# Performance work log

Hardware: AMD Instinct MI355X
Metric: run time of the kernel (lower is better)

The kernel has to match this reference:

```python
import jax, jax.numpy as jnp
import numpy as np

B, L, R, D = 4, 1024, 4, 1024   # batch, seq, expansion rate, model dim
HEADS, HD, FF = 16, 64, 4096
EPS = 1e-6


def _static_alpha(layer_id):
    a0 = np.zeros((R, 1), np.float32)
    a0[layer_id % R, 0] = 1.0
    return jnp.asarray(np.concatenate([a0, np.eye(R, dtype=np.float32)], axis=1))  # [R, R+1]


def setup_inputs() -> dict:
    key = jax.random.key(0)
    ks = jax.random.split(key, 12)
    w = lambda k, shape, s=0.02: (jax.random.normal(k, shape, jnp.float32) * s)
    return {
        "H": jax.random.normal(ks[0], (B, L, R, D), jnp.float32),
        # attention hyper-connection (layer_id*2 = 0)
        "hc1_norm_w": jnp.ones((D,), jnp.float32),
        "hc1_alpha_fn": w(ks[1], (D, R + 1), 0.01),
        "hc1_beta_fn": w(ks[2], (D,), 0.01),
        "hc1_a_scale": jnp.full((1,), 0.01, jnp.float32),
        "hc1_b_scale": jnp.full((1,), 0.01, jnp.float32),
        "hc1_s_alpha": _static_alpha(0),
        "hc1_s_beta": jnp.ones((R,), jnp.float32),
        # attention
        "attn_norm_w": jnp.ones((D,), jnp.float32),
        "qkv_w": w(ks[3], (3 * D, D)),
        "out_w": w(ks[4], (D, D)),
        # ffn hyper-connection (layer_id*2+1 = 1)
        "hc2_norm_w": jnp.ones((D,), jnp.float32),
        "hc2_alpha_fn": w(ks[5], (D, R + 1), 0.01),
        "hc2_beta_fn": w(ks[6], (D,), 0.01),
        "hc2_a_scale": jnp.full((1,), 0.01, jnp.float32),
        "hc2_b_scale": jnp.full((1,), 0.01, jnp.float32),
        "hc2_s_alpha": _static_alpha(1),
        "hc2_s_beta": jnp.ones((R,), jnp.float32),
        # ffn
        "ffn_norm_w": jnp.ones((D,), jnp.float32),
        "fc1_w": w(ks[7], (FF, D)),
        "fc2_w": w(ks[8], (D, FF)),
    }


def _rms(x, weight):
    norm = jnp.sqrt(jnp.mean(x * x, axis=-1, keepdims=True))
    return weight * x / (norm + EPS)


def _width(Hm, norm_w, alpha_fn, beta_fn, a_scale, b_scale, s_alpha, s_beta):
    nh = _rms(Hm, norm_w)                                      # [B,L,R,D]
    alpha = jnp.tanh(jnp.einsum('blnd,dk->blnk', nh, alpha_fn)) * a_scale + s_alpha  # [B,L,R,R+1]
    beta = jnp.tanh(jnp.einsum('blnd,d->bln', nh, beta_fn)) * b_scale + s_beta       # [B,L,R]
    mix = jnp.einsum('blnk,blnd->blkd', alpha, Hm)             # [B,L,R+1,D]
    return mix, beta


def _depth(mix, out, beta):
    return beta[..., None] * out[:, :, None, :] + mix[..., 1:, :]


def _attention(x, qkv_w, out_w):
    b, l, d = x.shape
    qkv = (x @ qkv_w.T).reshape(b, l, 3, HEADS, HD)
    q, k, v = (jnp.moveaxis(qkv, 2, 0)[i].transpose(0, 2, 1, 3) for i in range(3))  # [B,H,L,HD]
    scores = jnp.einsum('bhqd,bhkd->bhqk', q, k) * (HD ** -0.5)
    causal = jnp.tril(jnp.ones((l, l), bool))
    scores = jnp.where(causal, scores, jnp.float32(-jnp.inf))
    attn = jax.nn.softmax(scores, axis=-1)
    out = jnp.einsum('bhqk,bhkd->bhqd', attn, v).transpose(0, 2, 1, 3).reshape(b, l, d)
    return out @ out_w.T


def reference(H, hc1_norm_w, hc1_alpha_fn, hc1_beta_fn, hc1_a_scale, hc1_b_scale,
              hc1_s_alpha, hc1_s_beta, attn_norm_w, qkv_w, out_w,
              hc2_norm_w, hc2_alpha_fn, hc2_beta_fn, hc2_a_scale, hc2_b_scale,
              hc2_s_alpha, hc2_s_beta, ffn_norm_w, fc1_w, fc2_w):
    # attention block
    mix, beta = _width(H, hc1_norm_w, hc1_alpha_fn, hc1_beta_fn,
                       hc1_a_scale, hc1_b_scale, hc1_s_alpha, hc1_s_beta)
    h = _rms(mix[..., 0, :], attn_norm_w)
    h = _attention(h, qkv_w, out_w)
    H = _depth(mix, h, beta)
    # ffn block
    mix, beta = _width(H, hc2_norm_w, hc2_alpha_fn, hc2_beta_fn,
                       hc2_a_scale, hc2_b_scale, hc2_s_alpha, hc2_s_beta)
    h = _rms(mix[..., 0, :], ffn_norm_w)
    h = (jax.nn.gelu(h @ fc1_w.T, approximate=False)) @ fc2_w.T
    H = _depth(mix, h, beta)
    return H
```

## Files before the change

### kernel.cpp

```cpp
#include <hip/hip_runtime.h>
#include <math.h>

#define BB 4
#define LL 1024
#define RR 4
#define DD 1024
#define NHEADS 16
#define HDIM 64
#define FFD 4096
#define EPSV 1e-6f

typedef short s16x8 __attribute__((ext_vector_type(8)));
typedef float f32x4 __attribute__((ext_vector_type(4)));
typedef unsigned short u16;

__device__ inline unsigned short f2bf(float x) {
  unsigned u = __builtin_bit_cast(unsigned, x);
  unsigned r = (u + 0x7fffu + ((u >> 16) & 1u)) >> 16;
  return (unsigned short)r;
}
__device__ inline float bf2f(u16 x) {
  return __builtin_bit_cast(float, (unsigned)x << 16);
}

__device__ inline float wred_sum(float v) {
#pragma unroll
  for (int off = 32; off; off >>= 1) v += __shfl_down(v, off);
  return v;
}

__device__ inline void gload_lds16(const u16* g, u16* l) {
  __builtin_amdgcn_global_load_lds(
      (const __attribute__((address_space(1))) unsigned int*)g,
      (__attribute__((address_space(3))) unsigned int*)l, 16, 0, 0);
}

__global__ __launch_bounds__(256) void cvt4_kernel(
    const float* __restrict__ s0, const float* __restrict__ s1,
    const float* __restrict__ s2, const float* __restrict__ s3,
    u16* __restrict__ d0, u16* __restrict__ d1,
    u16* __restrict__ d2, u16* __restrict__ d3) {
  const int n0 = 786432, n1 = 262144, n2 = 1048576, n3 = 1048576;
  const int total = n0 + n1 + n2 + n3;
  for (int i = blockIdx.x * 256 + threadIdx.x; i < total; i += gridDim.x * 256) {
    const float4* src; ushort4* dst; int j;
    if (i < n0)                { src = (const float4*)s0; dst = (ushort4*)d0; j = i; }
    else if (i < n0 + n1)      { src = (const float4*)s1; dst = (ushort4*)d1; j = i - n0; }
    else if (i < n0 + n1 + n2) { src = (const float4*)s2; dst = (ushort4*)d2; j = i - n0 - n1; }
    else                       { src = (const float4*)s3; dst = (ushort4*)d3; j = i - n0 - n1 - n2; }
    float4 v = src[j];
    ushort4 o;
    o.x = f2bf(v.x); o.y = f2bf(v.y); o.z = f2bf(v.z); o.w = f2bf(v.w);
    dst[j] = o;
  }
}

template<int NP>
__global__ __launch_bounds__(256) void width_kernel(
    const float* __restrict__ Hin,
    const u16* mixrest_in,
    const float* __restrict__ beta_in,
    const u16* __restrict__ pp,
    const float* __restrict__ hc_norm_w,
    const float* __restrict__ alpha_fn,
    const float* __restrict__ beta_fn,
    const float* __restrict__ a_scale,
    const float* __restrict__ b_scale,
    const float* __restrict__ s_alpha,
    const float* __restrict__ s_beta,
    const float* __restrict__ post_norm_w,
    u16* mixrest_out,
    float* __restrict__ beta_out,
    u16* __restrict__ x_out)
{
  const size_t MN = (size_t)4096 * 1024;
  const int bl = blockIdx.x;
  const int t = threadIdx.x;
  const int wid = t >> 6;
  __shared__ __align__(16) float Hs[4 * 1024];
  __shared__ __align__(16) float m0[1024];
  __shared__ float scr[96];
  __shared__ float alpha_s[4][5];
  __shared__ float beta_s[4];
  __shared__ float inv_s[4];
  __shared__ float inv0_s;

  if (NP > 0) {
    int d0 = t * 4;
    float4 s; s.x = 0.f; s.y = 0.f; s.z = 0.f; s.w = 0.f;
#pragma unroll
    for (int p = 0; p < (NP > 0 ? NP : 1); ++p) {
      ushort4 v = *(const ushort4*)&pp[p * MN + (size_t)bl * 1024 + d0];
      s.x += bf2f(v.x); s.y += bf2f(v.y); s.z += bf2f(v.z); s.w += bf2f(v.w);
    }
    ((float4*)m0)[t] = s;
    __syncthreads();
    for (int i = t; i < 1024; i += 256) {
      int n = i >> 8;
      float be = beta_in[bl * 4 + n];
      ushort4 mr = ((const ushort4*)(mixrest_in + (size_t)bl * 4096))[i];
      float4 ao = ((const float4*)m0)[i & 255];
      float4 hv;
      hv.x = be * ao.x + bf2f(mr.x); hv.y = be * ao.y + bf2f(mr.y);
      hv.z = be * ao.z + bf2f(mr.z); hv.w = be * ao.w + bf2f(mr.w);
      ((float4*)Hs)[i] = hv;
    }
  } else {
    for (int i = t; i < 1024; i += 256)
      ((float4*)Hs)[i] = ((const float4*)(Hin + (size_t)bl * 4096))[i];
  }
  __syncthreads();

  float ss[4];
#pragma unroll
  for (int n = 0; n < 4; ++n) {
    float a = 0.f;
    for (int d = t; d < 1024; d += 256) { float v = Hs[n * 1024 + d]; a += v * v; }
    ss[n] = a;
  }
#pragma unroll
  for (int n = 0; n < 4; ++n) {
    float r = wred_sum(ss[n]);
    if ((t & 63) == 0) scr[wid * 4 + n] = r;
  }
  __syncthreads();
  if (t < 4) {
    float tot = scr[t] + scr[4 + t] + scr[8 + t] + scr[12 + t];
    inv_s[t] = 1.f / (sqrtf(tot * (1.f / 1024.f)) + EPSV);
  }
  __syncthreads();
  float inv[4] = {inv_s[0], inv_s[1], inv_s[2], inv_s[3]};

  float dots[4][6];
#pragma unroll
  for (int n = 0; n < 4; ++n)
#pragma unroll
    for (int k = 0; k < 6; ++k) dots[n][k] = 0.f;
  for (int d = t; d < 1024; d += 256) {
    float w = hc_norm_w[d];
    float a0 = alpha_fn[d * 5 + 0], a1 = alpha_fn[d * 5 + 1], a2 = alpha_fn[d * 5 + 2],
          a3 = alpha_fn[d * 5 + 3], a4 = alpha_fn[d * 5 + 4];
    float bfv = beta_fn[d];
#pragma unroll
    for (int n = 0; n < 4; ++n) {
      float nh = Hs[n * 1024 + d] * w * inv[n];
      dots[n][0] += nh * a0; dots[n][1] += nh * a1; dots[n][2] += nh * a2;
      dots[n][3] += nh * a3; dots[n][4] += nh * a4; dots[n][5] += nh * bfv;
    }
  }
  __syncthreads();
#pragma unroll
  for (int n = 0; n < 4; ++n)
#pragma unroll
    for (int k = 0; k < 6; ++k) {
      float r = wred_sum(dots[n][k]);
      if ((t & 63) == 0) scr[wid * 24 + n * 6 + k] = r;
    }
  __syncthreads();
  if (t < 24) {
    float raw = scr[t] + scr[24 + t] + scr[48 + t] + scr[72 + t];
    int n = t / 6, k = t % 6;
    if (k < 5) alpha_s[n][k] = tanhf(raw) * a_scale[0] + s_alpha[n * 5 + k];
    else       beta_s[n]     = tanhf(raw) * b_scale[0] + s_beta[n];
  }
  __syncthreads();

  {
    int i = t;
    float4 h0 = ((const float4*)Hs)[i];
    float4 h1 = ((const float4*)Hs)[256 + i];
    float4 h2 = ((const float4*)Hs)[512 + i];
    float4 h3 = ((const float4*)Hs)[768 + i];
#pragma unroll
    for (int k = 0; k < 5; ++k) {
      float c0 = alpha_s[0][k], c1 = alpha_s[1][k], c2 = alpha_s[2][k], c3 = alpha_s[3][k];
      float4 mv;
      mv.x = c0 * h0.x + c1 * h1.x + c2 * h2.x + c3 * h3.x;
      mv.y = c0 * h0.y + c1 * h1.y + c2 * h2.y + c3 * h3.y;
      mv.z = c0 * h0.z + c1 * h1.z + c2 * h2.z + c3 * h3.z;
      mv.w = c0 * h0.w + c1 * h1.w + c2 * h2.w + c3 * h3.w;
      if (k == 0) {
        ((float4*)m0)[i] = mv;
      } else {
        ushort4 ov;
        ov.x = f2bf(mv.x); ov.y = f2bf(mv.y); ov.z = f2bf(mv.z); ov.w = f2bf(mv.w);
        ((ushort4*)(mixrest_out + (size_t)bl * 4096 + (size_t)(k - 1) * 1024))[i] = ov;
      }
    }
  }
  if (t < 4) beta_out[bl * 4 + t] = beta_s[t];
  __syncthreads();

  {
    float a = 0.f;
    for (int d = t; d < 1024; d += 256) { float v = m0[d]; a += v * v; }
    float r = wred_sum(a);
    if ((t & 63) == 0) scr[wid] = r;
  }
  __syncthreads();
  if (t == 0) {
    float tot = scr[0] + scr[1] + scr[2] + scr[3];
    inv0_s = 1.f / (sqrtf(tot * (1.f / 1024.f)) + EPSV);
  }
  __syncthreads();
  {
    float iv = inv0_s;
    float4 mv = ((const float4*)m0)[t];
    float4 wv = ((const float4*)post_norm_w)[t];
    ushort4 ov;
    ov.x = f2bf(wv.x * mv.x * iv);
    ov.y = f2bf(wv.y * mv.y * iv);
    ov.z = f2bf(wv.z * mv.z * iv);
    ov.w = f2bf(wv.w * mv.w * iv);
    ((ushort4*)(x_out + (size_t)bl * 1024))[t] = ov;
  }
}

template<int EPI, int SPLIT>
__global__ __launch_bounds__(256, 4) void gemm_bt_kernel(
    const u16* __restrict__ A, const u16* __restrict__ W,
    u16* __restrict__ Cb, u16* __restrict__ Vt,
    int M, int N, int K)
{
  __shared__ __align__(16) u16 LDSb[2][2][128 * 32];
  const int tn = N >> 7, tm = M >> 7;
  int bid = blockIdx.x;
  const int nwg = gridDim.x;
  if ((nwg & 7) == 0) bid = (bid & 7) * (nwg >> 3) + (bid >> 3);
  const int ts = tm * tn;
  const int sK = bid / ts;
  const int tb = bid - sK * ts;
  const int bm = tb / tn, bn = tb % tn;
  const int Kc = K / SPLIT;
  const int kbeg = sK * Kc;

  const int t = threadIdx.x, l = t & 63, w = t >> 6;
  const int wr = w >> 1, wc = w & 1;
  const int m0 = bm << 7, n0 = bn << 7;
  const int ssc = (((l & 3) ^ ((l >> 3) & 3)) << 3);
  const int srA = m0 + (w << 5) + (l >> 2);
  const int srB = n0 + (w << 5) + (l >> 2);
  const int ldso = (w << 10);
  const int fr = l & 15, g4 = l >> 4;
  const int fc8 = ((g4 ^ ((l >> 1) & 3)) << 3);

  f32x4 acc[4][4];
#pragma unroll
  for (int i = 0; i < 4; ++i)
#pragma unroll
    for (int j = 0; j < 4; ++j)
#pragma unroll
      for (int e = 0; e < 4; ++e) acc[i][j][e] = 0.f;

  const u16* pa0 = A + (size_t)srA * K + kbeg + ssc;
  const u16* pa1 = A + (size_t)(srA + 16) * K + kbeg + ssc;
  const u16* pb0 = W + (size_t)srB * K + kbeg + ssc;
  const u16* pb1 = W + (size_t)(srB + 16) * K + kbeg + ssc;

#define STAGE(buf, koff)                                   \
  do {                                                     \
    gload_lds16(pa0 + (koff), &LDSb[buf][0][ldso]);        \
    gload_lds16(pa1 + (koff), &LDSb[buf][0][ldso + 512]);  \
    gload_lds16(pb0 + (koff), &LDSb[buf][1][ldso]);        \
    gload_lds16(pb1 + (koff), &LDSb[buf][1][ldso + 512]);  \
  } while (0)

  const int nt = Kc >> 5;
  STAGE(0, 0);
  int cur = 0;
  for (int kt = 0; kt < nt; ++kt) {
    if (kt + 1 < nt) {
      STAGE(cur ^ 1, (kt + 1) << 5);
      asm volatile("s_waitcnt vmcnt(4)" ::: "memory");
    } else {
      asm volatile("s_waitcnt vmcnt(0)" ::: "memory");
    }
    __builtin_amdgcn_s_barrier();
    __builtin_amdgcn_sched_barrier(0);
    s16x8 af[4], bfr[4];
#pragma unroll
    for (int m = 0; m < 4; ++m)
      af[m] = *(const s16x8*)(&LDSb[cur][0][(wr * 64 + m * 16 + fr) * 32 + fc8]);
#pragma unroll
    for (int n = 0; n < 4; ++n)
      bfr[n] = *(const s16x8*)(&LDSb[cur][1][(wc * 64 + n * 16 + fr) * 32 + fc8]);
#pragma unroll
    for (int m = 0; m < 4; ++m)
#pragma unroll
      for (int n = 0; n < 4; ++n)
        acc[m][n] = __builtin_amdgcn_mfma_f32_16x16x32_bf16(af[m], bfr[n], acc[m][n], 0, 0, 0);
    asm volatile("s_waitcnt lgkmcnt(0)" ::: "memory");
    __builtin_amdgcn_sched_barrier(0);
    __builtin_amdgcn_s_barrier();
    cur ^= 1;
  }
#undef STAGE

  if (EPI == 2 && n0 >= 2048) {
    const int rbv = m0 + wr * 64 + (g4 << 2);
    const int cbv = n0 + wc * 64 + fr;
#pragma unroll
    for (int m = 0; m < 4; ++m)
#pragma unroll
      for (int n = 0; n < 4; ++n) {
        int cc = cbv + n * 16 - 2048;
        int hh = cc >> 6, dd = cc & 63;
        int r0 = rbv + m * 16;
        ushort4 ov;
        ov.x = f2bf(acc[m][n][0]); ov.y = f2bf(acc[m][n][1]);
        ov.z = f2bf(acc[m][n][2]); ov.w = f2bf(acc[m][n][3]);
        *(ushort4*)&Vt[((size_t)((r0 >> 10) * 16 + hh) * 64 + dd) * 1024 + (r0 & 1023)] = ov;
      }
    return;
  }

  float* scr = (float*)LDSb;
  const int strideN = (EPI == 2) ? 2048 : N;
  u16* Cout = (SPLIT > 1) ? (Cb + (size_t)sK * M * N) : Cb;
#pragma unroll
  for (int r = 0; r < 2; ++r) {
    __syncthreads();
    if (wr == r) {
#pragma unroll
      for (int m = 0; m < 4; ++m)
#pragma unroll
        for (int n = 0; n < 4; ++n)
#pragma unroll
          for (int j = 0; j < 4; ++j) {
            int lr = m * 16 + (g4 << 2) + j;
            int col = wc * 64 + n * 16 + fr;
            scr[lr * 128 + (col ^ ((((lr >> 2) & 7)) << 3))] = acc[m][n][j];
          }
    }
    __syncthreads();
#pragma unroll
    for (int it = 0; it < 4; ++it) {
      int lr = it * 16 + (t >> 4);
      int key8 = ((lr >> 2) & 7) << 3;
      int lc = (t & 15) << 3;
      int cb0 = (lc ^ key8);
      f32x4 v0 = *(const f32x4*)&scr[lr * 128 + cb0];
      f32x4 v1 = *(const f32x4*)&scr[lr * 128 + cb0 + 4];
      float vv[8] = {v0[0], v0[1], v0[2], v0[3], v1[0], v1[1], v1[2], v1[3]};
      s16x8 ov;
#pragma unroll
      for (int c = 0; c < 8; ++c) {
        float v = vv[c];
        if (EPI == 1) v = 0.5f * v * (1.f + erff(v * 0.70710678118f));
        ov[c] = (short)f2bf(v);
      }
      size_t gr = (size_t)(m0 + r * 64 + lr);
      *(s16x8*)&Cout[gr * strideN + n0 + lc] = ov;
    }
  }
}

__global__ __launch_bounds__(256) void attn_mfma_kernel(
    const u16* __restrict__ qk, const u16* __restrict__ Vt, u16* __restrict__ out)
{
  const int h = blockIdx.y, b = blockIdx.z;
  const int qt = (h & 1) ? (15 - blockIdx.x) : blockIdx.x;
  const int t = threadIdx.x, l = t & 63, w = t >> 6;
  const int q0 = qt << 6;
  __shared__ __align__(16) u16 Ks[64 * 64];
  __shared__ __align__(16) u16 Vs[64 * 64];
  __shared__ __align__(16) u16 Ps[4][16 * 64];

  const int fr = l & 15;
  const int fg = (l >> 4) << 3;
  const int fswz = (fr & 7) << 3;

  const int qrow = q0 + w * 16 + fr;
  const size_t qbase = (size_t)(b * 1024 + qrow) * 2048 + h * 64 + fg;
  const s16x8 aq0 = *(const s16x8*)(qk + qbase);
  const s16x8 aq1 = *(const s16x8*)(qk + qbase + 32);

  f32x4 acc_o[4];
#pragma unroll
  for (int i = 0; i < 4; ++i)
#pragma unroll
    for (int e = 0; e < 4; ++e) acc_o[i][e] = 0.f;
  float m_i[4] = {-INFINITY, -INFINITY, -INFINITY, -INFINITY};
  float l_i[4] = {0.f, 0.f, 0.f, 0.f};

  const int srow = t >> 2;
  const int sc = (t & 3) << 4;
  const int c0s = sc ^ ((srow & 7) << 3);
  const int c1s = (sc + 8) ^ ((srow & 7) << 3);
  const int qrow_c = q0 + w * 16 + ((l >> 4) << 2);
  u16* Psw = &Ps[w][0];
  const int nkt = qt + 1;

  for (int kt = 0; kt < nkt; ++kt) {
    const int kb = kt << 6;
    __syncthreads();
    {
      size_t kg = (size_t)(b * 1024 + kb + srow) * 2048 + 1024 + h * 64 + sc;
      s16x8 kv0 = *(const s16x8*)(qk + kg);
      s16x8 kv1 = *(const s16x8*)(qk + kg + 8);
      size_t vg = (size_t)((b * 16 + h) * 64 + srow) * 1024 + kb + sc;
      s16x8 vv0 = *(const s16x8*)(Vt + vg);
      s16x8 vv1 = *(const s16x8*)(Vt + vg + 8);
      *(s16x8*)(Ks + srow * 64 + c0s) = kv0;
      *(s16x8*)(Ks + srow * 64 + c1s) = kv1;
      *(s16x8*)(Vs + srow * 64 + c0s) = vv0;
      *(s16x8*)(Vs + srow * 64 + c1s) = vv1;
    }
    __syncthreads();

    f32x4 s[4];
#pragma unroll
    for (int n = 0; n < 4; ++n) {
#pragma unroll
      for (int e = 0; e < 4; ++e) s[n][e] = 0.f;
      s16x8 bk0 = *(const s16x8*)(Ks + (n * 16 + fr) * 64 + (fg ^ fswz));
      s16x8 bk1 = *(const s16x8*)(Ks + (n * 16 + fr) * 64 + ((32 + fg) ^ fswz));
      s[n] = __builtin_amdgcn_mfma_f32_16x16x32_bf16(aq0, bk0, s[n], 0, 0, 0);
      s[n] = __builtin_amdgcn_mfma_f32_16x16x32_bf16(aq1, bk1, s[n], 0, 0, 0);
    }
#pragma unroll
    for (int n = 0; n < 4; ++n)
#pragma unroll
      for (int e = 0; e < 4; ++e) s[n][e] *= 0.125f;
    if (kt == qt) {
#pragma unroll
      for (int n = 0; n < 4; ++n) {
        int kc = kb + n * 16 + fr;
#pragma unroll
        for (int r = 0; r < 4; ++r)
          if (kc > qrow_c + r) s[n][r] = -INFINITY;
      }
    }

    float rm[4], fac[4];
#pragma unroll
    for (int r = 0; r < 4; ++r)
      rm[r] = fmaxf(fmaxf(s[0][r], s[1][r]), fmaxf(s[2][r], s[3][r]));
#pragma unroll
    for (int off = 1; off < 16; off <<= 1)
#pragma unroll
      for (int r = 0; r < 4; ++r) rm[r] = fmaxf(rm[r], __shfl_xor(rm[r], off));
#pragma unroll
    for (int r = 0; r < 4; ++r) {
      float mn = fmaxf(m_i[r], rm[r]);
      fac[r] = __expf(m_i[r] - mn);
      m_i[r] = mn;
    }
    float rs[4] = {0.f, 0.f, 0.f, 0.f};
    float pb[4][4];
#pragma unroll
    for (int n = 0; n < 4; ++n)
#pragma unroll
      for (int r = 0; r < 4; ++r) {
        float pv = __expf(s[n][r] - m_i[r]);
        pb[n][r] = pv;
        rs[r] += pv;
      }
#pragma unroll
    for (int off = 1; off < 16; off <<= 1)
#pragma unroll
      for (int r = 0; r < 4; ++r) rs[r] += __shfl_xor(rs[r], off);
#pragma unroll
    for (int r = 0; r < 4; ++r) l_i[r] = l_i[r] * fac[r] + rs[r];
#pragma unroll
    for (int dt = 0; dt < 4; ++dt)
#pragma unroll
      for (int r = 0; r < 4; ++r) acc_o[dt][r] *= fac[r];

#pragma unroll
    for (int n = 0; n < 4; ++n)
#pragma unroll
      for (int r = 0; r < 4; ++r) {
        int prow = ((l >> 4) << 2) + r;
        Psw[prow * 64 + ((n * 16 + fr) ^ ((prow & 7) << 3))] = f2bf(pb[n][r]);
      }
    asm volatile("s_waitcnt lgkmcnt(0)" ::: "memory");
    __builtin_amdgcn_sched_barrier(0);

    s16x8 pa0 = *(const s16x8*)(Psw + fr * 64 + (fg ^ fswz));
    s16x8 pa1 = *(const s16x8*)(Psw + fr * 64 + ((32 + fg) ^ fswz));
#pragma unroll
    for (int dt = 0; dt < 4; ++dt) {
      s16x8 bv0 = *(const s16x8*)(Vs + (dt * 16 + fr) * 64 + (fg ^ fswz));
      s16x8 bv1 = *(const s16x8*)(Vs + (dt * 16 + fr) * 64 + ((32 + fg) ^ fswz));
      acc_o[dt] = __builtin_amdgcn_mfma_f32_16x16x32_bf16(pa0, bv0, acc_o[dt], 0, 0, 0);
      acc_o[dt] = __builtin_amdgcn_mfma_f32_16x16x32_bf16(pa1, bv1, acc_o[dt], 0, 0, 0);
    }
  }

  float invl[4];
#pragma unroll
  for (int r = 0; r < 4; ++r) invl[r] = 1.f / l_i[r];
#pragma unroll
  for (int dt = 0; dt < 4; ++dt)
#pragma unroll
    for (int r = 0; r < 4; ++r) {
      size_t idx = (size_t)(b * 1024 + qrow_c + r) * 1024 + h * 64 + dt * 16 + fr;
      out[idx] = f2bf(acc_o[dt][r] * invl[r]);
    }
}

template<int NPART>
__global__ __launch_bounds__(256) void depth2_kernel(
    const u16* __restrict__ parts, const u16* __restrict__ mixrest,
    const float* __restrict__ beta, float* __restrict__ Hout)
{
  const size_t MN = (size_t)4096 * 1024;
  const size_t stride = (size_t)gridDim.x * 256;
  const size_t n8 = (size_t)BB * LL * RR * DD / 8;
  for (size_t i = (size_t)blockIdx.x * 256 + threadIdx.x; i < n8; i += stride) {
    size_t e = i * 8;
    int d = (int)(e & 1023);
    int n = (int)((e >> 10) & 3);
    size_t bl = e >> 12;
    float be = beta[bl * 4 + n];
    float f[8];
#pragma unroll
    for (int j = 0; j < 8; ++j) f[j] = 0.f;
#pragma unroll
    for (int p = 0; p < NPART; ++p) {
      s16x8 v = *(const s16x8*)&parts[p * MN + bl * 1024 + d];
#pragma unroll
      for (int j = 0; j < 8; ++j) f[j] += bf2f((u16)v[j]);
    }
    s16x8 m = *(const s16x8*)&mixrest[e];
    float4 o0, o1;
    o0.x = be * f[0] + bf2f((u16)m[0]); o0.y = be * f[1] + bf2f((u16)m[1]);
    o0.z = be * f[2] + bf2f((u16)m[2]); o0.w = be * f[3] + bf2f((u16)m[3]);
    o1.x = be * f[4] + bf2f((u16)m[4]); o1.y = be * f[5] + bf2f((u16)m[5]);
    o1.z = be * f[6] + bf2f((u16)m[6]); o1.w = be * f[7] + bf2f((u16)m[7]);
    *(float4*)&Hout[e] = o0;
    *(float4*)&Hout[e + 4] = o1;
  }
}

extern "C" void kernel_launch(void* const* d_in, const int* in_sizes, int n_in,
                              void* d_out, int out_size, void* d_ws, size_t ws_size,
                              hipStream_t stream) {
  const float* H       = (const float*)d_in[0];
  const float* hc1_nw  = (const float*)d_in[1];
  const float* hc1_afn = (const float*)d_in[2];
  const float* hc1_bfn = (const float*)d_in[3];
  const float* hc1_as  = (const float*)d_in[4];
  const float* hc1_bs  = (const float*)d_in[5];
  const float* hc1_sa  = (const float*)d_in[6];
  const float* hc1_sb  = (const float*)d_in[7];
  const float* attn_nw = (const float*)d_in[8];
  const float* qkv_w   = (const float*)d_in[9];
  const float* out_w   = (const float*)d_in[10];
  const float* hc2_nw  = (const float*)d_in[11];
  const float* hc2_afn = (const float*)d_in[12];
  const float* hc2_bfn = (const float*)d_in[13];
  const float* hc2_as  = (const float*)d_in[14];
  const float* hc2_bs  = (const float*)d_in[15];
  const float* hc2_sa  = (const float*)d_in[16];
  const float* hc2_sb  = (const float*)d_in[17];
  const float* ffn_nw  = (const float*)d_in[18];
  const float* fc1_w   = (const float*)d_in[19];
  const float* fc2_w   = (const float*)d_in[20];
  float* Hout = (float*)d_out;

  char* wsp = (char*)d_ws;
  size_t off = 0;
  auto carve = [&](size_t bytes) {
    void* p = wsp + off;
    off = (off + bytes + 255) & ~(size_t)255;
    return p;
  };
  const size_t MN = (size_t)4096 * 1024;
  u16* wq_bf   = (u16*)carve((size_t)3072 * 1024 * 2);
  u16* wo_bf   = (u16*)carve((size_t)1024 * 1024 * 2);
  u16* w1_bf   = (u16*)carve((size_t)4096 * 1024 * 2);
  u16* w2_bf   = (u16*)carve((size_t)4096 * 1024 * 2);
  u16* xbf     = (u16*)carve((size_t)4096 * 1024 * 2);
  u16* mixrest = (u16*)carve((size_t)4096 * 4096 * 2);
  float* beta1 = (float*)carve((size_t)16384 * 4);
  float* beta2 = (float*)carve((size_t)16384 * 4);
  char* uregion = (char*)carve((size_t)32 * 1024 * 1024);
  u16* qk_bf   = (u16*)uregion;
  u16* Vt      = (u16*)(uregion + (size_t)16 * 1024 * 1024);
  u16* g1_bf   = (u16*)uregion;
  u16* attn_bf = (u16*)carve((size_t)4096 * 1024 * 2);
  u16* pp      = (u16*)carve((size_t)4 * MN * 2);

  cvt4_kernel<<<2048, 256, 0, stream>>>(qkv_w, out_w, fc1_w, fc2_w, wq_bf, wo_bf, w1_bf, w2_bf);
  width_kernel<0><<<4096, 256, 0, stream>>>(H, nullptr, nullptr, nullptr,
      hc1_nw, hc1_afn, hc1_bfn, hc1_as, hc1_bs, hc1_sa, hc1_sb, attn_nw,
      mixrest, beta1, xbf);
  gemm_bt_kernel<2, 1><<<768, 256, 0, stream>>>(xbf, wq_bf, qk_bf, Vt, 4096, 3072, 1024);
  attn_mfma_kernel<<<dim3(16, 16, 4), 256, 0, stream>>>(qk_bf, Vt, attn_bf);
  gemm_bt_kernel<0, 4><<<1024, 256, 0, stream>>>(attn_bf, wo_bf, pp, nullptr, 4096, 1024, 1024);
  width_kernel<4><<<4096, 256, 0, stream>>>(nullptr, mixrest, beta1, pp,
      hc2_nw, hc2_afn, hc2_bfn, hc2_as, hc2_bs, hc2_sa, hc2_sb, ffn_nw,
      mixrest, beta2, xbf);
  gemm_bt_kernel<1, 1><<<1024, 256, 0, stream>>>(xbf, w1_bf, g1_bf, nullptr, 4096, 4096, 1024);
  gemm_bt_kernel<0, 4><<<1024, 256, 0, stream>>>(g1_bf, w2_bf, pp, nullptr, 4096, 1024, 4096);
  depth2_kernel<4><<<4096, 256, 0, stream>>>(pp, mixrest, beta2, Hout);
}
```

Measured before the change: 351.5 us.

## Load K and V fragments directly from global memory in attention, drop LDS staging

The attention kernel no longer stages K and V tiles through shared memory with two block barriers per key tile. Each wave now loads its MFMA B-operand fragments for K and V straight from global memory, and V loads are issued early so they can overlap the softmax. This removes the barriers and LDS traffic. In exchange, each of the four waves fetches the same K/V data redundantly from global memory or cache, and loads are more scattered.

```diff
diff --git a/kernel.cpp b/kernel.cpp
--- a/kernel.cpp
+++ b/kernel.cpp
@@ -362,8 +362,6 @@
   const int qt = (h & 1) ? (15 - blockIdx.x) : blockIdx.x;
   const int t = threadIdx.x, l = t & 63, w = t >> 6;
   const int q0 = qt << 6;
-  __shared__ __align__(16) u16 Ks[64 * 64];
-  __shared__ __align__(16) u16 Vs[64 * 64];
   __shared__ __align__(16) u16 Ps[4][16 * 64];
 
   const int fr = l & 15;
@@ -375,6 +373,9 @@
   const s16x8 aq0 = *(const s16x8*)(qk + qbase);
   const s16x8 aq1 = *(const s16x8*)(qk + qbase + 32);
 
+  const u16* kbase = qk + (size_t)(b * 1024 + fr) * 2048 + 1024 + h * 64 + fg;
+  const u16* vbase = Vt + ((size_t)((b * 16 + h) * 64 + fr)) * 1024 + fg;
+
   f32x4 acc_o[4];
 #pragma unroll
   for (int i = 0; i < 4; ++i)
@@ -383,41 +384,33 @@
   float m_i[4] = {-INFINITY, -INFINITY, -INFINITY, -INFINITY};
   float l_i[4] = {0.f, 0.f, 0.f, 0.f};
 
-  const int srow = t >> 2;
-  const int sc = (t & 3) << 4;
-  const int c0s = sc ^ ((srow & 7) << 3);
-  const int c1s = (sc + 8) ^ ((srow & 7) << 3);
   const int qrow_c = q0 + w * 16 + ((l >> 4) << 2);
   u16* Psw = &Ps[w][0];
   const int nkt = qt + 1;
 
   for (int kt = 0; kt < nkt; ++kt) {
     const int kb = kt << 6;
-    __syncthreads();
-    {
-      size_t kg = (size_t)(b * 1024 + kb + srow) * 2048 + 1024 + h * 64 + sc;
-      s16x8 kv0 = *(const s16x8*)(qk + kg);
-      s16x8 kv1 = *(const s16x8*)(qk + kg + 8);
-      size_t vg = (size_t)((b * 16 + h) * 64 + srow) * 1024 + kb + sc;
-      s16x8 vv0 = *(const s16x8*)(Vt + vg);
-      s16x8 vv1 = *(const s16x8*)(Vt + vg + 8);
-      *(s16x8*)(Ks + srow * 64 + c0s) = kv0;
-      *(s16x8*)(Ks + srow * 64 + c1s) = kv1;
-      *(s16x8*)(Vs + srow * 64 + c0s) = vv0;
-      *(s16x8*)(Vs + srow * 64 + c1s) = vv1;
-    }
-    __syncthreads();
 
     f32x4 s[4];
 #pragma unroll
     for (int n = 0; n < 4; ++n) {
 #pragma unroll
       for (int e = 0; e < 4; ++e) s[n][e] = 0.f;
-      s16x8 bk0 = *(const s16x8*)(Ks + (n * 16 + fr) * 64 + (fg ^ fswz));
-      s16x8 bk1 = *(const s16x8*)(Ks + (n * 16 + fr) * 64 + ((32 + fg) ^ fswz));
+      const u16* kp = kbase + (size_t)(kb + n * 16) * 2048;
+      s16x8 bk0 = *(const s16x8*)(kp);
+      s16x8 bk1 = *(const s16x8*)(kp + 32);
       s[n] = __builtin_amdgcn_mfma_f32_16x16x32_bf16(aq0, bk0, s[n], 0, 0, 0);
       s[n] = __builtin_amdgcn_mfma_f32_16x16x32_bf16(aq1, bk1, s[n], 0, 0, 0);
     }
+
+    s16x8 bv0[4], bv1[4];
+#pragma unroll
+    for (int dt = 0; dt < 4; ++dt) {
+      const u16* vp = vbase + (size_t)(dt * 16) * 1024 + kb;
+      bv0[dt] = *(const s16x8*)(vp);
+      bv1[dt] = *(const s16x8*)(vp + 32);
+    }
+
 #pragma unroll
     for (int n = 0; n < 4; ++n)
 #pragma unroll
@@ -481,10 +474,8 @@
     s16x8 pa1 = *(const s16x8*)(Psw + fr * 64 + ((32 + fg) ^ fswz));
 #pragma unroll
     for (int dt = 0; dt < 4; ++dt) {
-      s16x8 bv0 = *(const s16x8*)(Vs + (dt * 16 + fr) * 64 + (fg ^ fswz));
-      s16x8 bv1 = *(const s16x8*)(Vs + (dt * 16 + fr) * 64 + ((32 + fg) ^ fswz));
-      acc_o[dt] = __builtin_amdgcn_mfma_f32_16x16x32_bf16(pa0, bv0, acc_o[dt], 0, 0, 0);
-      acc_o[dt] = __builtin_amdgcn_mfma_f32_16x16x32_bf16(pa1, bv1, acc_o[dt], 0, 0, 0);
+      acc_o[dt] = __builtin_amdgcn_mfma_f32_16x16x32_bf16(pa0, bv0[dt], acc_o[dt], 0, 0, 0);
+      acc_o[dt] = __builtin_amdgcn_mfma_f32_16x16x32_bf16(pa1, bv1[dt], acc_o[dt], 0, 0, 0);
     }
   }
 
```

Result: slower. 399.2 us (+13.6%).
